# Kernel optimization log

Hardware: AMD Instinct MI355X
Metric: run time of the kernel (lower is better)

The kernel has to match this reference:

```python
import jax, jax.numpy as jnp
import numpy as np

N_QUBITS = 8


def _cnot_perm(n, c, t):
    idx = np.arange(2 ** n)
    cbit = (idx >> (n - 1 - c)) & 1
    return np.where(cbit == 1, idx ^ (1 << (n - 1 - t)), idx)

CNOT_PERMS = [jnp.asarray(_cnot_perm(N_QUBITS, q, (q + 1) % N_QUBITS)) for q in range(N_QUBITS)]


def _apply_1q(state, q, U):
    # state: (N, 2^n) complex; U: (2,2) shared or (N,2,2) per-token
    N = state.shape[0]
    s = state.reshape(N, 2 ** q, 2, -1)
    if U.ndim == 2:
        s = jnp.einsum('ab,nibj->niaj', U, s)
    else:
        s = jnp.einsum('nab,nibj->niaj', U, s)
    return s.reshape(N, -1)


def _ry(theta):
    c, s = jnp.cos(theta / 2), jnp.sin(theta / 2)
    return jnp.stack([jnp.stack([c, -s], -1), jnp.stack([s, c], -1)], -2).astype(jnp.complex64)


def _rz(theta):
    e = jnp.exp(0.5j * theta.astype(jnp.complex64))
    z = jnp.zeros_like(e)
    return jnp.stack([jnp.stack([jnp.conj(e), z], -1), jnp.stack([z, e], -1)], -2)


def _quantum_states(x, theta):
    # x: (N, n_qubits) encoding angles; theta: (L, n_qubits, 2)
    N, n = x.shape
    state = jnp.zeros((N, 2 ** n), jnp.complex64).at[:, 0].set(1.0)
    for q in range(n):  # RY angle encoding
        state = _apply_1q(state, q, _ry(x[:, q]))
    for l in range(theta.shape[0]):  # variational layers
        for q in range(n):
            state = _apply_1q(state, q, _ry(theta[l, q, 0]))
            state = _apply_1q(state, q, _rz(theta[l, q, 1]))
        for q in range(n):  # ring entangler CNOT(q, q+1)
            state = state[:, CNOT_PERMS[q]]
    return state


def setup_inputs() -> dict:
    key = jax.random.key(0)
    ks = jax.random.split(key, 8)
    B, S, E, n, L = 128, 128, 1024, N_QUBITS, 4
    return {
        'X': jax.random.normal(ks[0], (B, S, E), jnp.float32),
        'Wi': jax.random.normal(ks[1], (E, n), jnp.float32) * 0.02,
        'bi': jnp.zeros((n,), jnp.float32),
        'Wv': jax.random.normal(ks[2], (E, E), jnp.float32) * 0.02,
        'bv': jnp.zeros((E,), jnp.float32),
        'Wo': jax.random.normal(ks[3], (E, E), jnp.float32) * 0.02,
        'bo': jnp.zeros((E,), jnp.float32),
        'theta': jax.random.normal(ks[4], (L, n, 2), jnp.float32) * 0.1,
        'phi': jax.random.normal(ks[5], (S,), jnp.float32) * 0.1,
    }


def reference(X, Wi, bi, Wv, bv, Wo, bo, theta, phi):
    B, S, E = X.shape
    qin = X @ Wi + bi          # (B,S,n_qubits)
    V = X @ Wv + bv            # (B,S,E)
    psi = _quantum_states(qin.reshape(B * S, -1), theta).reshape(B, S, -1)
    G = jnp.einsum('bsd,btd->bst', psi, jnp.conj(psi))  # overlaps
    K = (G.real ** 2 + G.imag ** 2) / jnp.sqrt(jnp.float32(N_QUBITS))
    phi_s = phi[:S]
    K = K + jnp.cos(phi_s[None, :] - phi_s[:, None])    # cosine positional bias
    attn = jax.nn.softmax(K, axis=-1)                   # (B,S,S)
    out = jnp.einsum('bst,bte->bse', attn, V)
    y = out @ Wo + bo
    return y, attn
```

## Files before the change

### kernel.cpp

```cpp
#include <hip/hip_runtime.h>
#include <hip/hip_bf16.h>

#define BB 128
#define SS 128
#define EE 1024
#define NQ 8
#define DD 256
#define LL 4
#define MM (BB*SS)

typedef unsigned short bf16s;
typedef __attribute__((ext_vector_type(8))) short bf16x8;
typedef __attribute__((ext_vector_type(4))) float f32x4;

#define AS1 __attribute__((address_space(1)))
#define AS3 __attribute__((address_space(3)))

__device__ __forceinline__ unsigned short f2bf(float x) {
    unsigned u = __float_as_uint(x);
    u += 0x7fffu + ((u >> 16) & 1u);
    return (unsigned short)(u >> 16);
}

#define PIPE_WAIT(N) do { \
    asm volatile("s_waitcnt vmcnt(" #N ")" ::: "memory"); \
    __builtin_amdgcn_sched_barrier(0); \
    __builtin_amdgcn_s_barrier(); \
    __builtin_amdgcn_sched_barrier(0); } while (0)
#define PIPE_BAR() do { \
    __builtin_amdgcn_sched_barrier(0); \
    __builtin_amdgcn_s_barrier(); } while (0)

__global__ __launch_bounds__(256) void transpose_conv_kernel(
    const float* __restrict__ in, bf16s* __restrict__ out, int R, int C)
{
    __shared__ float t[32][33];
    int bx = blockIdx.x * 32, by = blockIdx.y * 32;
    int lx = threadIdx.x & 31, ly = threadIdx.x >> 5;
#pragma unroll
    for (int i = 0; i < 32; i += 8)
        t[ly + i][lx] = in[(size_t)(by + ly + i) * C + bx + lx];
    __syncthreads();
#pragma unroll
    for (int i = 0; i < 32; i += 8)
        out[(size_t)(bx + ly + i) * R + by + lx] = f2bf(t[lx][ly + i]);
}

__global__ __launch_bounds__(256) void cvt_kernel(
    const float* __restrict__ in, bf16s* __restrict__ out)
{
    int g = blockIdx.x * 256 + threadIdx.x;
    f32x4 x = ((const f32x4*)in)[g];
    ushort4 o;
    o.x = f2bf(x[0]); o.y = f2bf(x[1]); o.z = f2bf(x[2]); o.w = f2bf(x[3]);
    ((ushort4*)out)[g] = o;
}

__global__ __launch_bounds__(256) void bvo_part_kernel(
    const float* __restrict__ bv, const float* __restrict__ Wo,
    float* __restrict__ part)
{
    __shared__ float red[4][64];
    int lane = threadIdx.x & 63, w = threadIdx.x >> 6;
    int eb = blockIdx.x & 15, kb = blockIdx.x >> 4;
    int e = eb * 64 + lane;
    int k0 = kb * 64 + w * 16;
    float acc = 0.f;
#pragma unroll
    for (int i = 0; i < 16; i++)
        acc += bv[k0 + i] * Wo[(size_t)(k0 + i) * EE + e];
    red[w][lane] = acc;
    __syncthreads();
    if (w == 0)
        part[kb * EE + e] = red[0][lane] + red[1][lane] + red[2][lane] + red[3][lane];
}

__global__ __launch_bounds__(256) void bvo_reduce_kernel(
    const float* __restrict__ part, const float* __restrict__ bo,
    float* __restrict__ bvo)
{
    int e = blockIdx.x * 256 + threadIdx.x;
    float s = bo[e];
#pragma unroll
    for (int kb = 0; kb < 16; kb++) s += part[kb * EE + e];
    bvo[e] = s;
}

__global__ __launch_bounds__(256) void wtrans_kernel(
    const float* __restrict__ Wi, float* __restrict__ Wit)
{
    int g = blockIdx.x * 256 + threadIdx.x;
    int k = g >> 3, j = g & 7;
    Wit[j * 1024 + k] = Wi[g];
}

__global__ __launch_bounds__(256) void encode_kernel(
    const float* __restrict__ X, const float* __restrict__ Wit,
    const float* __restrict__ bi,
    bf16s* __restrict__ Xb, bf16s* __restrict__ v)
{
    const int lane = threadIdx.x & 63;
    const int wid  = threadIdx.x >> 6;
    const int row0 = blockIdx.x * 16 + wid * 4;

    f32x4 wreg[8][4];
#pragma unroll
    for (int j = 0; j < 8; j++)
#pragma unroll
        for (int t = 0; t < 4; t++)
            wreg[j][t] = ((const f32x4*)(Wit + j * 1024))[t * 64 + lane];

    float bis[8];
#pragma unroll
    for (int j = 0; j < 8; j++) bis[j] = bi[j];

    f32x4 xa0, xa1, xa2, xa3, xn0, xn1, xn2, xn3;
    {
        const f32x4* xr = (const f32x4*)(X + (size_t)row0 * EE);
        xa0 = xr[0 * 64 + lane]; xa1 = xr[1 * 64 + lane];
        xa2 = xr[2 * 64 + lane]; xa3 = xr[3 * 64 + lane];
    }

#pragma unroll
    for (int rr = 0; rr < 4; rr++) {
        const int row = row0 + rr;
        if (rr < 3) {
            const f32x4* xn = (const f32x4*)(X + (size_t)(row + 1) * EE);
            xn0 = xn[0 * 64 + lane]; xn1 = xn[1 * 64 + lane];
            xn2 = xn[2 * 64 + lane]; xn3 = xn[3 * 64 + lane];
        }

        ushort4* xbr4 = (ushort4*)(Xb + (size_t)row * EE);
        float acc[8];
#pragma unroll
        for (int j = 0; j < 8; j++) acc[j] = 0.f;

        f32x4 xs[4] = {xa0, xa1, xa2, xa3};
#pragma unroll
        for (int t = 0; t < 4; t++) {
            f32x4 x = xs[t];
            ushort4 xb;
            xb.x = f2bf(x[0]); xb.y = f2bf(x[1]);
            xb.z = f2bf(x[2]); xb.w = f2bf(x[3]);
            xbr4[t * 64 + lane] = xb;
#pragma unroll
            for (int j = 0; j < 8; j++) {
                f32x4 w = wreg[j][t];
                acc[j] += x[0]*w[0] + x[1]*w[1] + x[2]*w[2] + x[3]*w[3];
            }
        }

        float qin[8];
#pragma unroll
        for (int j = 0; j < 8; j++) {
            float s = acc[j];
#pragma unroll
            for (int off = 32; off >= 1; off >>= 1) s += __shfl_xor(s, off, 64);
            qin[j] = s + bis[j];
        }

        float cs[8], sn[8];
#pragma unroll
        for (int q = 0; q < 8; q++) __sincosf(0.5f * qin[q], &sn[q], &cs[q]);

        float common = 1.f;
#pragma unroll
        for (int b = 2; b < 8; b++) {
            int q = 7 - b;
            common *= ((lane >> (b - 2)) & 1) ? sn[q] : cs[q];
        }
        float a0 = common * cs[6] * cs[7];
        float a1 = common * cs[6] * sn[7];
        float a2 = common * sn[6] * cs[7];
        float a3 = common * sn[6] * sn[7];
        ushort4 vo;
        vo.x = f2bf(a0); vo.y = f2bf(a1); vo.z = f2bf(a2); vo.w = f2bf(a3);
        ((ushort4*)(v + (size_t)row * DD))[lane] = vo;

        xa0 = xn0; xa1 = xn1; xa2 = xn2; xa3 = xn3;
    }
}

__global__ __launch_bounds__(512) void gemm256_kernel(
    const bf16s* __restrict__ A, const bf16s* __restrict__ Bt,
    bf16s* __restrict__ C, int M, int N, int K, int nm, int nn)
{
    extern __shared__ bf16s lds[];
    bf16s* As = lds;
    bf16s* Bs = lds + 4 * 8192;

    const int tid  = threadIdx.x;
    const int lane = tid & 63;
    const int wid  = tid >> 6;
    const int quad = lane >> 4, lr = lane & 15;
    const int wr = wid >> 2, wc = wid & 3;

    const int nwg = gridDim.x;
    const int q = nwg >> 3, r = nwg & 7;
    const int xcd = blockIdx.x & 7, idx = blockIdx.x >> 3;
    const int w = (xcd < r ? xcd * (q + 1) : r * (q + 1) + (xcd - r) * q) + idx;
    const int m_t = w % nm, n_t = w / nm;
    const int m0 = m_t * 256, n0 = n_t * 256;

    f32x4 acc[8][4];
#pragma unroll
    for (int i = 0; i < 8; i++)
#pragma unroll
        for (int j = 0; j < 4; j++) acc[i][j] = (f32x4){0.f, 0.f, 0.f, 0.f};

    auto stage = [&](int slot, int kt) {
#pragma unroll
        for (int l = 0; l < 2; l++) {
            int ch = l * 512 + tid;
            int row = ch >> 2;
            int kc = ((ch & 3) ^ (row & 3)) * 8;
            __builtin_amdgcn_global_load_lds(
                (AS1 const void*)(A + (size_t)(m0 + row) * K + kt * 32 + kc),
                (AS3 void*)(As + slot * 8192 + ch * 8), 16, 0, 0);
        }
#pragma unroll
        for (int l = 0; l < 2; l++) {
            int ch = l * 512 + tid;
            int row = ch >> 2;
            int kc = ((ch & 3) ^ (row & 3)) * 8;
            __builtin_amdgcn_global_load_lds(
                (AS1 const void*)(Bt + (size_t)(n0 + row) * K + kt * 32 + kc),
                (AS3 void*)(Bs + slot * 8192 + ch * 8), 16, 0, 0);
        }
    };
    auto compute = [&](int slot) {
        bf16x8 af[8];
#pragma unroll
        for (int i = 0; i < 8; i++) {
            int rowl = wr * 128 + i * 16 + lr;
            af[i] = *(const bf16x8*)(As + slot * 8192 + rowl * 32
                                     + ((quad ^ (rowl & 3)) * 8));
        }
#pragma unroll
        for (int j = 0; j < 4; j++) {
            int rowl = wc * 64 + j * 16 + lr;
            bf16x8 bfr = *(const bf16x8*)(Bs + slot * 8192 + rowl * 32
                                          + ((quad ^ (rowl & 3)) * 8));
#pragma unroll
            for (int i = 0; i < 8; i++)
                acc[i][j] = __builtin_amdgcn_mfma_f32_16x16x32_bf16(
                    af[i], bfr, acc[i][j], 0, 0, 0);
        }
    };

    const int NT = K >> 5;
    stage(0, 0);
    stage(1, 1);
    for (int kt = 0; kt < NT; kt++) {
        if (kt + 1 < NT) PIPE_WAIT(4);
        else             PIPE_WAIT(0);
        if (kt + 2 < NT) stage((kt + 2) & 3, kt + 2);
        compute(kt & 3);
    }

#pragma unroll
    for (int i = 0; i < 8; i++) {
        int row0 = m0 + wr * 128 + i * 16 + quad * 4;
#pragma unroll
        for (int j = 0; j < 4; j++) {
            int col = n0 + wc * 64 + j * 16 + lr;
#pragma unroll
            for (int rr = 0; rr < 4; rr++)
                C[(size_t)(row0 + rr) * N + col] = f2bf(acc[i][j][rr]);
        }
    }
}

template<bool OUT_BF16>
__global__ __launch_bounds__(256) void mfma_gemm(
    const bf16s* __restrict__ A, const bf16s* __restrict__ Bt,
    const float* __restrict__ bias, void* __restrict__ Cv,
    int M, int N, int K, int ldB, int nm, int nn,
    long long sA, long long sB, long long sC)
{
    __shared__ bf16s As[3][128 * 32];
    __shared__ bf16s Bs[3][128 * 32];

    const int tid  = threadIdx.x;
    const int wave = tid >> 6, lane = tid & 63;
    const int quad = lane >> 4, lr = lane & 15;
    const int wm = (wave >> 1) * 64, wn = (wave & 1) * 64;

    const int nwg = gridDim.x;
    const int q = nwg >> 3, r = nwg & 7;
    const int xcd = blockIdx.x & 7, idx = blockIdx.x >> 3;
    const int w = (xcd < r ? xcd * (q + 1) : r * (q + 1) + (xcd - r) * q) + idx;
    const int n_t = w % nn;
    const int m_t = (w / nn) % nm;
    const int z   = w / (nn * nm);
    const int m0 = m_t * 128, n0 = n_t * 128;

    A  += (size_t)z * sA;
    Bt += (size_t)z * sB;

    f32x4 acc[4][4];
#pragma unroll
    for (int i = 0; i < 4; i++)
#pragma unroll
        for (int j = 0; j < 4; j++) acc[i][j] = (f32x4){0.f, 0.f, 0.f, 0.f};

    auto stage = [&](int buf, int kt) {
#pragma unroll
        for (int j = 0; j < 2; j++) {
            int ch = j * 256 + tid;
            int row = ch >> 2, kc = (ch & 3) * 8;
            __builtin_amdgcn_global_load_lds(
                (AS1 const void*)(A + (size_t)(m0 + row) * K + kt + kc),
                (AS3 void*)(As[buf] + (size_t)(j * 256 + wave * 64) * 8), 16, 0, 0);
            __builtin_amdgcn_global_load_lds(
                (AS1 const void*)(Bt + (size_t)(n0 + row) * ldB + kt + kc),
                (AS3 void*)(Bs[buf] + (size_t)(j * 256 + wave * 64) * 8), 16, 0, 0);
        }
    };
    auto compute = [&](int buf) {
        bf16x8 af[4], bfr[4];
#pragma unroll
        for (int i = 0; i < 4; i++)
            af[i] = *(const bf16x8*)(As[buf] + (wm + i * 16 + lr) * 32 + quad * 8);
#pragma unroll
        for (int j = 0; j < 4; j++)
            bfr[j] = *(const bf16x8*)(Bs[buf] + (wn + j * 16 + lr) * 32 + quad * 8);
#pragma unroll
        for (int i = 0; i < 4; i++)
#pragma unroll
            for (int j = 0; j < 4; j++)
                acc[i][j] = __builtin_amdgcn_mfma_f32_16x16x32_bf16(
                    af[i], bfr[j], acc[i][j], 0, 0, 0);
    };

    const int nt = K >> 5;
    stage(0, 0);
    stage(1, 1 << 5);
    int cur = 0, nxt = 2;
    for (int t = 0; t < nt; t++) {
        if (t + 2 < nt) { stage(nxt, (t + 2) << 5); PIPE_WAIT(8); }
        else if (t + 1 < nt) PIPE_WAIT(4);
        else PIPE_WAIT(0);
        compute(cur);
        PIPE_BAR();
        cur = (cur == 2) ? 0 : cur + 1;
        nxt = (nxt == 2) ? 0 : nxt + 1;
    }

    float* Cf = (float*)Cv + (size_t)z * sC;
    bf16s* Cb = (bf16s*)Cv + (size_t)z * sC;
#pragma unroll
    for (int i = 0; i < 4; i++) {
        int row0 = m0 + wm + i * 16 + quad * 4;
#pragma unroll
        for (int j = 0; j < 4; j++) {
            int col = n0 + wn + j * 16 + lr;
            float bb = bias ? bias[col] : 0.f;
#pragma unroll
            for (int r = 0; r < 4; r++) {
                float v = acc[i][j][r] + bb;
                if (OUT_BF16) Cb[(size_t)(row0 + r) * N + col] = f2bf(v);
                else          Cf[(size_t)(row0 + r) * N + col] = v;
            }
        }
    }
}

__global__ __launch_bounds__(256) void attn_kernel(
    const bf16s* __restrict__ v, const float* __restrict__ phi,
    float* __restrict__ attn, bf16s* __restrict__ attn_bf)
{
    __shared__ bf16s Bs[3][128 * 32];

    const int tid  = threadIdx.x;
    const int wave = tid >> 6, lane = tid & 63;
    const int quad = lane >> 4, lr = lane & 15;
    const int b = blockIdx.y;
    const int s0 = blockIdx.x * 64;
    const bf16s* vb = v + (size_t)b * 128 * DD;

    f32x4 accre[8];
#pragma unroll
    for (int j = 0; j < 8; j++) accre[j] = (f32x4){0.f, 0.f, 0.f, 0.f};

    auto stage = [&](int buf, int kt) {
#pragma unroll
        for (int j = 0; j < 2; j++) {
            int ch = j * 256 + tid;
            int row = ch >> 2, kc = (ch & 3) * 8;
            __builtin_amdgcn_global_load_lds(
                (AS1 const void*)(vb + (size_t)row * DD + kt + kc),
                (AS3 void*)(Bs[buf] + (size_t)(j * 256 + wave * 64) * 8), 16, 0, 0);
        }
    };
    auto compute = [&](int buf) {
        bf16x8 afr = *(const bf16x8*)(Bs[buf] + (s0 + wave * 16 + lr) * 32 + quad * 8);
#pragma unroll
        for (int j = 0; j < 8; j++) {
            bf16x8 b1 = *(const bf16x8*)(Bs[buf] + (j * 16 + lr) * 32 + quad * 8);
            accre[j] = __builtin_amdgcn_mfma_f32_16x16x32_bf16(afr, b1, accre[j], 0, 0, 0);
        }
    };

    const int nt = DD >> 5;
    stage(0, 0);
    stage(1, 1 << 5);
    int cur = 0, nxt = 2;
    for (int t = 0; t < nt; t++) {
        if (t + 2 < nt) { stage(nxt, (t + 2) << 5); PIPE_WAIT(4); }
        else if (t + 1 < nt) PIPE_WAIT(2);
        else PIPE_WAIT(0);
        compute(cur);
        PIPE_BAR();
        cur = (cur == 2) ? 0 : cur + 1;
        nxt = (nxt == 2) ? 0 : nxt + 1;
    }

    const float isq = 0.35355339059327373f;
    float ph_r[4], ph_c[8];
#pragma unroll
    for (int r = 0; r < 4; r++) ph_r[r] = phi[s0 + wave * 16 + quad * 4 + r];
#pragma unroll
    for (int j = 0; j < 8; j++) ph_c[j] = phi[j * 16 + lr];

#pragma unroll
    for (int r = 0; r < 4; r++) {
        float vv[8];
        float mx = -1e30f;
#pragma unroll
        for (int j = 0; j < 8; j++) {
            float re = accre[j][r];
            vv[j] = re * re * isq + __cosf(ph_c[j] - ph_r[r]);
            mx = fmaxf(mx, vv[j]);
        }
#pragma unroll
        for (int off = 1; off <= 8; off <<= 1) mx = fmaxf(mx, __shfl_xor(mx, off, 64));
        float sm = 0.f;
#pragma unroll
        for (int j = 0; j < 8; j++) { vv[j] = __expf(vv[j] - mx); sm += vv[j]; }
#pragma unroll
        for (int off = 1; off <= 8; off <<= 1) sm += __shfl_xor(sm, off, 64);
        float inv = 1.f / sm;
        int srow = b * 128 + s0 + wave * 16 + quad * 4 + r;
#pragma unroll
        for (int j = 0; j < 8; j++) {
            float o = vv[j] * inv;
            attn[(size_t)srow * 128 + j * 16 + lr] = o;
            attn_bf[(size_t)srow * 128 + j * 16 + lr] = f2bf(o);
        }
    }
}

extern "C" void kernel_launch(void* const* d_in, const int* in_sizes, int n_in,
                              void* d_out, int out_size, void* d_ws, size_t ws_size,
                              hipStream_t stream) {
    const float* X     = (const float*)d_in[0];
    const float* Wi    = (const float*)d_in[1];
    const float* bi    = (const float*)d_in[2];
    const float* Wv    = (const float*)d_in[3];
    const float* bv    = (const float*)d_in[4];
    const float* Wo    = (const float*)d_in[5];
    const float* bo    = (const float*)d_in[6];
    const float* phi   = (const float*)d_in[8];

    float* y    = (float*)d_out;
    float* attn = y + (size_t)MM * EE;

    bf16s* Xb   = (bf16s*)d_ws;
    bf16s* Vwt  = Xb  + (size_t)MM * EE;
    bf16s* v    = Vwt + (size_t)MM * EE;
    bf16s* abf  = v   + (size_t)MM * DD;
    bf16s* Wvb  = abf + (size_t)BB * SS * SS;
    bf16s* Wot  = Wvb + (size_t)EE * EE;
    bf16s* Wvot = Wot + (size_t)EE * EE;
    float* Wit  = (float*)(Wvot + (size_t)EE * EE);
    float* bvo  = Wit + 8 * 1024;
    float* bvop = bvo + 1024;

    wtrans_kernel<<<32, 256, 0, stream>>>(Wi, Wit);
    encode_kernel<<<MM / 16, 256, 0, stream>>>(X, Wit, bi, Xb, v);
    transpose_conv_kernel<<<dim3(32, 32), 256, 0, stream>>>(Wo, Wot, EE, EE);
    cvt_kernel<<<1024, 256, 0, stream>>>(Wv, Wvb);
    bvo_part_kernel<<<256, 256, 0, stream>>>(bv, Wo, bvop);
    bvo_reduce_kernel<<<4, 256, 0, stream>>>(bvop, bo, bvo);
    mfma_gemm<true><<<64, 256, 0, stream>>>(
        Wot, Wvb, nullptr, Wvot, EE, EE, EE, EE, 8, 8, 0, 0, 0);
    attn_kernel<<<dim3(2, BB), 256, 0, stream>>>(v, phi, attn, abf);
    gemm256_kernel<<<256, 512, 128 * 1024, stream>>>(
        Wvot, Xb, Vwt, EE, MM, EE, 4, 64);
    mfma_gemm<false><<<1024, 256, 0, stream>>>(
        abf, Vwt, bvo, y, SS, EE, SS, MM, 1, 8,
        (long long)SS * SS, (long long)SS, (long long)SS * EE);
}
```

Baseline: 246.3 us.

## Split GEMM k-step into two interleaved load/MFMA phases with priority hints

```diff
diff --git a/kernel.cpp b/kernel.cpp
--- a/kernel.cpp
+++ b/kernel.cpp
@@ -30,6 +30,9 @@
 #define PIPE_BAR() do { \
     __builtin_amdgcn_sched_barrier(0); \
     __builtin_amdgcn_s_barrier(); } while (0)
+#define LGKM0_FENCE() do { \
+    asm volatile("s_waitcnt lgkmcnt(0)" ::: "memory"); \
+    __builtin_amdgcn_sched_barrier(0); } while (0)
 
 __global__ __launch_bounds__(256) void transpose_conv_kernel(
     const float* __restrict__ in, bf16s* __restrict__ out, int R, int C)
@@ -208,7 +211,7 @@
 #pragma unroll
         for (int j = 0; j < 4; j++) acc[i][j] = (f32x4){0.f, 0.f, 0.f, 0.f};
 
-    auto stage = [&](int slot, int kt) {
+    auto stageA = [&](int slot, int kt) {
 #pragma unroll
         for (int l = 0; l < 2; l++) {
             int ch = l * 512 + tid;
@@ -218,6 +221,8 @@
                 (AS1 const void*)(A + (size_t)(m0 + row) * K + kt * 32 + kc),
                 (AS3 void*)(As + slot * 8192 + ch * 8), 16, 0, 0);
         }
+    };
+    auto stageB = [&](int slot, int kt) {
 #pragma unroll
         for (int l = 0; l < 2; l++) {
             int ch = l * 512 + tid;
@@ -228,34 +233,59 @@
                 (AS3 void*)(Bs + slot * 8192 + ch * 8), 16, 0, 0);
         }
     };
-    auto compute = [&](int slot) {
-        bf16x8 af[8];
-#pragma unroll
-        for (int i = 0; i < 8; i++) {
-            int rowl = wr * 128 + i * 16 + lr;
-            af[i] = *(const bf16x8*)(As + slot * 8192 + rowl * 32
-                                     + ((quad ^ (rowl & 3)) * 8));
-        }
-#pragma unroll
-        for (int j = 0; j < 4; j++) {
-            int rowl = wc * 64 + j * 16 + lr;
-            bf16x8 bfr = *(const bf16x8*)(Bs + slot * 8192 + rowl * 32
-                                          + ((quad ^ (rowl & 3)) * 8));
-#pragma unroll
-            for (int i = 0; i < 8; i++)
-                acc[i][j] = __builtin_amdgcn_mfma_f32_16x16x32_bf16(
-                    af[i], bfr, acc[i][j], 0, 0, 0);
-        }
-    };
 
     const int NT = K >> 5;
-    stage(0, 0);
-    stage(1, 1);
+    stageA(0, 0); stageB(0, 0);
+    stageA(1, 1); stageB(1, 1);
+
     for (int kt = 0; kt < NT; kt++) {
         if (kt + 1 < NT) PIPE_WAIT(4);
         else             PIPE_WAIT(0);
-        if (kt + 2 < NT) stage((kt + 2) & 3, kt + 2);
-        compute(kt & 3);
+
+        const int slot = kt & 3;
+        const bf16s* Asl = As + slot * 8192;
+        const bf16s* Bsl = Bs + slot * 8192;
+
+        bf16x8 af[8], bfr[4];
+#pragma unroll
+        for (int i = 0; i < 4; i++) {
+            int rowl = wr * 128 + i * 16 + lr;
+            af[i] = *(const bf16x8*)(Asl + rowl * 32 + ((quad ^ (rowl & 3)) * 8));
+        }
+#pragma unroll
+        for (int j = 0; j < 4; j++) {
+            int rowl = wc * 64 + j * 16 + lr;
+            bfr[j] = *(const bf16x8*)(Bsl + rowl * 32 + ((quad ^ (rowl & 3)) * 8));
+        }
+        if (kt + 2 < NT) stageA((kt + 2) & 3, kt + 2);
+        PIPE_BAR();
+        LGKM0_FENCE();
+        __builtin_amdgcn_s_setprio(1);
+#pragma unroll
+        for (int i = 0; i < 4; i++)
+#pragma unroll
+            for (int j = 0; j < 4; j++)
+                acc[i][j] = __builtin_amdgcn_mfma_f32_16x16x32_bf16(
+                    af[i], bfr[j], acc[i][j], 0, 0, 0);
+        __builtin_amdgcn_s_setprio(0);
+        PIPE_BAR();
+
+#pragma unroll
+        for (int i = 4; i < 8; i++) {
+            int rowl = wr * 128 + i * 16 + lr;
+            af[i] = *(const bf16x8*)(Asl + rowl * 32 + ((quad ^ (rowl & 3)) * 8));
+        }
+        if (kt + 2 < NT) stageB((kt + 2) & 3, kt + 2);
+        PIPE_BAR();
+        LGKM0_FENCE();
+        __builtin_amdgcn_s_setprio(1);
+#pragma unroll
+        for (int i = 4; i < 8; i++)
+#pragma unroll
+            for (int j = 0; j < 4; j++)
+                acc[i][j] = __builtin_amdgcn_mfma_f32_16x16x32_bf16(
+                    af[i], bfr[j], acc[i][j], 0, 0, 0);
+        __builtin_amdgcn_s_setprio(0);
     }
 
 #pragma unroll
```

After: 248.2 us. No clear change (+0.8%).
